# Optimization experiments

Measured on AMD Instinct MI355X. Metric: run time of the kernel, lower is better.

The kernel has to match this reference:

```python
import jax, jax.numpy as jnp
import numpy as np

B, S, H = 2, 2048, 2048
NH, NKV, HD = 16, 4, 128
NEG = -1e9


def rotate_half(x):
    x1, x2 = x[..., : x.shape[-1] // 2], x[..., x.shape[-1] // 2 :]
    return jnp.concatenate((-x2, x1), axis=-1)


def setup_inputs() -> dict:
    key = jax.random.key(0)
    ks = jax.random.split(key, 6)
    hidden_states = jax.random.normal(ks[0], (B, S, H), dtype=jnp.float32)
    # causal additive mask [B, 1, S, S]
    causal = jnp.tril(jnp.ones((S, S), dtype=bool))
    attention_mask = jnp.where(causal, 0.0, NEG).astype(jnp.float32)
    attention_mask = jnp.broadcast_to(attention_mask, (B, 1, S, S))
    # rotary embeddings, base 10000
    inv_freq = 1.0 / (10000.0 ** (np.arange(0, HD, 2, dtype=np.float32) / HD))
    pos = np.arange(S, dtype=np.float32)
    freqs = np.outer(pos, inv_freq)  # [S, HD/2]
    emb = np.concatenate([freqs, freqs], axis=-1)  # [S, HD]
    cos = jnp.broadcast_to(jnp.asarray(np.cos(emb)), (B, S, HD))
    sin = jnp.broadcast_to(jnp.asarray(np.sin(emb)), (B, S, HD))
    sc = 0.02
    Wq = jax.random.normal(ks[1], (H, NH * HD), dtype=jnp.float32) * sc
    Wk = jax.random.normal(ks[2], (H, NKV * HD), dtype=jnp.float32) * sc
    Wv = jax.random.normal(ks[3], (H, NKV * HD), dtype=jnp.float32) * sc
    Wo = jax.random.normal(ks[4], (H, H), dtype=jnp.float32) * sc
    return {"hidden_states": hidden_states, "attention_mask": attention_mask,
            "cos": cos, "sin": sin, "Wq": Wq, "Wk": Wk, "Wv": Wv, "Wo": Wo}


def reference(hidden_states, attention_mask, cos, sin, Wq, Wk, Wv, Wo):
    b, s, _ = hidden_states.shape
    # projections -> [b, heads, s, hd]
    q = (hidden_states @ Wq).reshape(b, s, NH, HD).transpose(0, 2, 1, 3)
    k = (hidden_states @ Wk).reshape(b, s, NKV, HD).transpose(0, 2, 1, 3)
    v = (hidden_states @ Wv).reshape(b, s, NKV, HD).transpose(0, 2, 1, 3)
    # RoPE (cos/sin unsqueezed at dim 1)
    c, sn = cos[:, None], sin[:, None]
    q = q * c + rotate_half(q) * sn
    k = k * c + rotate_half(k) * sn
    # GQA repeat_kv: [b, nkv, s, hd] -> [b, nh, s, hd]
    n_rep = NH // NKV
    k = jnp.repeat(k, n_rep, axis=1)
    v = jnp.repeat(v, n_rep, axis=1)
    scores = jnp.einsum("bhqd,bhkd->bhqk", q, k) / jnp.sqrt(jnp.float32(HD))
    scores = scores + attention_mask
    probs = jax.nn.softmax(scores.astype(jnp.float32), axis=-1).astype(q.dtype)
    out = jnp.einsum("bhqk,bhkd->bhqd", probs, v)
    out = out.transpose(0, 2, 1, 3).reshape(b, s, NH * HD)
    return out @ Wo
```

## Files before the change

kernel.cpp:

```cpp
#include <hip/hip_runtime.h>
#include <hip/hip_bf16.h>

typedef __bf16 bf16;
typedef __bf16 bf16x4 __attribute__((ext_vector_type(4)));
typedef __bf16 bf16x8 __attribute__((ext_vector_type(8)));
typedef float f32x4 __attribute__((ext_vector_type(4)));

__device__ __forceinline__ void gload_lds16(const void* g, void* l) {
  __builtin_amdgcn_global_load_lds((__attribute__((address_space(1))) void*)(g),
                                   (__attribute__((address_space(3))) void*)(l), 16, 0, 0);
}
__device__ __forceinline__ float fexp2(float x) {
  float r;
  asm volatile("v_exp_f32 %0, %1" : "=v"(r) : "v"(x));
  return r;
}

__global__ void k_diag(float* __restrict__ o, float v) { o[threadIdx.x] = v; }

__global__ void k_cvt_bf16(const float* __restrict__ x, bf16* __restrict__ y, int n4) {
  int i = blockIdx.x * blockDim.x + threadIdx.x;
  if (i < n4) {
    float4 v = reinterpret_cast<const float4*>(x)[i];
    bf16x4 o = {(bf16)v.x, (bf16)v.y, (bf16)v.z, (bf16)v.w};
    reinterpret_cast<bf16x4*>(y)[i] = o;
  }
}

__global__ void k_transpose_w(const float* __restrict__ W, bf16* __restrict__ Wt, int K, int N) {
  __shared__ float tile[32][33];
  int kb = blockIdx.x * 32, nb = blockIdx.y * 32;
  int tx = threadIdx.x & 31, ty = threadIdx.x >> 5;
#pragma unroll
  for (int i = 0; i < 32; i += 8)
    tile[ty + i][tx] = W[(size_t)(kb + ty + i) * N + nb + tx];
  __syncthreads();
#pragma unroll
  for (int i = 0; i < 32; i += 8)
    Wt[(size_t)(nb + ty + i) * K + kb + tx] = (bf16)tile[tx][ty + i];
}

__global__ void k_transpose_v(const bf16* __restrict__ KVb, bf16* __restrict__ Vt) {
  __shared__ bf16 tile[32][34];
  constexpr int S = 2048;
  int sb = blockIdx.x * 32, db = blockIdx.y * 32, bh = blockIdx.z;
  int b = bh >> 2, kvh = bh & 3;
  int tx = threadIdx.x & 31, ty = threadIdx.x >> 5;
  const bf16* src = KVb + (size_t)b * S * 1024 + 512 + kvh * 128;
#pragma unroll
  for (int i = 0; i < 32; i += 8)
    tile[ty + i][tx] = src[(size_t)(sb + ty + i) * 1024 + db + tx];
  __syncthreads();
  bf16* dst = Vt + (size_t)bh * 128 * S;
#pragma unroll
  for (int i = 0; i < 32; i += 8)
    dst[(size_t)(db + ty + i) * S + sb + tx] = tile[tx][ty + i];
}

template <typename OT>
__global__ __launch_bounds__(256) void k_gemm(const bf16* __restrict__ A, const bf16* __restrict__ Bt,
                                              OT* __restrict__ C, int M, int N, int Kd) {
  __shared__ __align__(16) bf16 sA[2][128 * 32];
  __shared__ __align__(16) bf16 sB[2][128 * 32];
  const int t = threadIdx.x;
  const int w = t >> 6, l = t & 63;
  const int lr = l & 15, lk = l >> 4;
  const int gx = gridDim.x, nwg = gx * gridDim.y;
  const int flat = blockIdx.y * gx + blockIdx.x;
  const int vid = (flat & 7) * (nwg >> 3) + (flat >> 3);
  const int m0 = (vid % gx) * 128, n0 = (vid / gx) * 128;
  const int wm = (w >> 1) * 64, wn = (w & 1) * 64;
  const bf16* ga = A + (size_t)(m0 + (t >> 2)) * Kd + (t & 3) * 8;
  const bf16* gb = Bt + (size_t)(n0 + (t >> 2)) * Kd + (t & 3) * 8;
  const size_t rowskip = (size_t)64 * Kd;
  auto stage = [&](int k0, int buf) {
    gload_lds16(ga + k0, sA[buf] + w * 512);
    gload_lds16(ga + rowskip + k0, sA[buf] + w * 512 + 2048);
    gload_lds16(gb + k0, sB[buf] + w * 512);
    gload_lds16(gb + rowskip + k0, sB[buf] + w * 512 + 2048);
  };
  f32x4 acc[4][4] = {};
  stage(0, 0);
  __syncthreads();
  int cur = 0;
  for (int k0 = 0; k0 < Kd; k0 += 32) {
    if (k0 + 32 < Kd) stage(k0 + 32, cur ^ 1);
    bf16x8 af[4], bfr[4];
#pragma unroll
    for (int i = 0; i < 4; ++i)
      af[i] = *reinterpret_cast<const bf16x8*>(sA[cur] + (wm + i * 16 + lr) * 32 + lk * 8);
#pragma unroll
    for (int j = 0; j < 4; ++j)
      bfr[j] = *reinterpret_cast<const bf16x8*>(sB[cur] + (wn + j * 16 + lr) * 32 + lk * 8);
#pragma unroll
    for (int i = 0; i < 4; ++i)
#pragma unroll
      for (int j = 0; j < 4; ++j)
        acc[i][j] = __builtin_amdgcn_mfma_f32_16x16x32_bf16(af[i], bfr[j], acc[i][j], 0, 0, 0);
    __syncthreads();
    cur ^= 1;
  }
#pragma unroll
  for (int i = 0; i < 4; ++i)
#pragma unroll
    for (int j = 0; j < 4; ++j)
#pragma unroll
      for (int r = 0; r < 4; ++r) {
        int row = m0 + wm + i * 16 + lk * 4 + r;
        int col = n0 + wn + j * 16 + lr;
        if constexpr (sizeof(OT) == 4)
          C[(size_t)row * N + col] = acc[i][j][r];
        else
          C[(size_t)row * N + col] = (bf16)acc[i][j][r];
      }
}

__global__ void k_rope(bf16* __restrict__ X, const float* __restrict__ cs, const float* __restrict__ sn,
                       int nh, int rowstride, float scale, int total) {
  int idx = blockIdx.x * blockDim.x + threadIdx.x;
  if (idx >= total) return;
  int d = idx & 63;
  int th = idx >> 6;
  int h = th % nh;
  int tok = th / nh;
  size_t base = (size_t)tok * rowstride + h * 128;
  float c = cs[tok * 128 + d], s = sn[tok * 128 + d];
  float x1 = (float)X[base + d];
  float x2 = (float)X[base + d + 64];
  X[base + d] = (bf16)((x1 * c - x2 * s) * scale);
  X[base + d + 64] = (bf16)((x2 * c + x1 * s) * scale);
}

__global__ __launch_bounds__(256) void k_attn(const bf16* __restrict__ Q, const bf16* __restrict__ KV,
                                              const bf16* __restrict__ Vt, bf16* __restrict__ O) {
  constexpr int S = 2048, NH = 16, HD = 128, QSTR = NH * HD, KVSTR = 1024;
  __shared__ __align__(16) bf16 sK[2][64 * 128];
  __shared__ __align__(16) bf16 sV[2][128 * 64];
  __shared__ __align__(16) bf16 sP[4][16][72];
  const int bid = blockIdx.x;
  const int vid = (bid & 7) * 64 + (bid >> 3);
  const int p = vid & 15, bh = vid >> 4;
  const int h = bh & 15, b = bh >> 4;
  const int t = threadIdx.x, w = t >> 6, l = t & 63;
  const int lr = l & 15, lk = l >> 4;
  const int kvh = h >> 2;
  const int swz = (lr & 7) << 4;

  const char* kbase = (const char*)(KV + (size_t)b * S * KVSTR + kvh * HD);
  const int krow_l = w * 16 + (l >> 4);
  const int kcol_l = (l & 15) << 4;
  const char* vtbase = (const char*)(Vt + (size_t)(b * 4 + kvh) * HD * S);
  const int vrow_l = w * 32 + (l >> 3);
  const int vcol_l = (l & 7) << 4;
  char* sKb = (char*)sK;
  char* sVb = (char*)sV;
  auto stage = [&](int kvb, int buf) {
#pragma unroll
    for (int c = 0; c < 4; ++c) {
      const int krow = krow_l + c * 4;
      gload_lds16(kbase + (size_t)(kvb + krow) * 2048 + (kcol_l ^ ((krow & 7) << 4)),
                  sKb + buf * 16384 + (w * 4 + c) * 1024);
      const int vrow = vrow_l + c * 8;
      gload_lds16(vtbase + (size_t)vrow * (S * 2) + kvb * 2 + (vcol_l ^ ((vrow & 7) << 4)),
                  sVb + buf * 16384 + (w * 4 + c) * 1024);
    }
  };

  for (int seg = 0; seg < 2; ++seg) {
    const int qtl = seg ? (31 - p) : p;
    const int qw = qtl * 64 + w * 16;
    const int ntiles = qtl + 1;
    int cur = 0;
    stage(0, 0);
    const bf16* Qp = Q + (size_t)(b * S + qw + lr) * QSTR + h * HD + lk * 8;
    bf16x8 qf[4];
#pragma unroll
    for (int i = 0; i < 4; ++i) qf[i] = *reinterpret_cast<const bf16x8*>(Qp + i * 32);
    f32x4 oacc[8] = {};
    float mrow[4] = {-3e38f, -3e38f, -3e38f, -3e38f};
    float lsum[4] = {0.f, 0.f, 0.f, 0.f};
    __syncthreads();
    for (int tt = 0; tt < ntiles; ++tt) {
      const int kvb = tt * 64;
      if (tt + 1 < ntiles) stage(kvb + 64, cur ^ 1);
      const char* sKc = sKb + cur * 16384;
      const char* sVc = sVb + cur * 16384;
      float pm[4][4];
#pragma unroll
      for (int c = 0; c < 4; ++c) {
        f32x4 s4 = {};
#pragma unroll
        for (int kf = 0; kf < 4; ++kf) {
          bf16x8 kf8 = *reinterpret_cast<const bf16x8*>(
              sKc + (c * 16 + lr) * 256 + (((kf * 64) + (lk << 4)) ^ swz));
          s4 = __builtin_amdgcn_mfma_f32_16x16x32_bf16(qf[kf], kf8, s4, 0, 0, 0);
        }
#pragma unroll
        for (int r = 0; r < 4; ++r) pm[c][r] = s4[r];
      }
      if (tt == ntiles - 1) {
#pragma unroll
        for (int c = 0; c < 4; ++c) {
          const int col = kvb + c * 16 + lr;
#pragma unroll
          for (int r = 0; r < 4; ++r)
            if (col > qw + lk * 4 + r) pm[c][r] = -3e38f;
        }
      }
      float pmax[4];
#pragma unroll
      for (int r = 0; r < 4; ++r)
        pmax[r] = fmaxf(fmaxf(pm[0][r], pm[1][r]), fmaxf(pm[2][r], pm[3][r]));
      bool hi = (pmax[0] > mrow[0] + 8.f) | (pmax[1] > mrow[1] + 8.f) |
                (pmax[2] > mrow[2] + 8.f) | (pmax[3] > mrow[3] + 8.f);
      if (__any(hi)) {
        float mx[4];
#pragma unroll
        for (int r = 0; r < 4; ++r) mx[r] = pmax[r];
#pragma unroll
        for (int off = 1; off < 16; off <<= 1)
#pragma unroll
          for (int r = 0; r < 4; ++r) mx[r] = fmaxf(mx[r], __shfl_xor(mx[r], off));
#pragma unroll
        for (int r = 0; r < 4; ++r) {
          float mn = fmaxf(mrow[r], mx[r]);
          float fac = fexp2(mrow[r] - mn);
          mrow[r] = mn;
          lsum[r] *= fac;
#pragma unroll
          for (int ch = 0; ch < 8; ++ch) oacc[ch][r] *= fac;
        }
      }
#pragma unroll
      for (int c = 0; c < 4; ++c)
#pragma unroll
        for (int r = 0; r < 4; ++r) pm[c][r] = fexp2(pm[c][r] - mrow[r]);
#pragma unroll
      for (int r = 0; r < 4; ++r)
        lsum[r] += (pm[0][r] + pm[1][r]) + (pm[2][r] + pm[3][r]);
#pragma unroll
      for (int c = 0; c < 4; ++c)
#pragma unroll
        for (int r = 0; r < 4; ++r) sP[w][lk * 4 + r][c * 16 + lr] = (bf16)pm[c][r];
      bf16x8 pf0 = *reinterpret_cast<const bf16x8*>(&sP[w][lr][lk * 8]);
      bf16x8 pf1 = *reinterpret_cast<const bf16x8*>(&sP[w][lr][32 + lk * 8]);
#pragma unroll
      for (int ch = 0; ch < 8; ++ch) {
        bf16x8 vf0 = *reinterpret_cast<const bf16x8*>(
            sVc + (ch * 16 + lr) * 128 + ((lk << 4) ^ swz));
        oacc[ch] = __builtin_amdgcn_mfma_f32_16x16x32_bf16(pf0, vf0, oacc[ch], 0, 0, 0);
        bf16x8 vf1 = *reinterpret_cast<const bf16x8*>(
            sVc + (ch * 16 + lr) * 128 + ((64 + (lk << 4)) ^ swz));
        oacc[ch] = __builtin_amdgcn_mfma_f32_16x16x32_bf16(pf1, vf1, oacc[ch], 0, 0, 0);
      }
      __syncthreads();
      cur ^= 1;
    }
#pragma unroll
    for (int off = 1; off < 16; off <<= 1)
#pragma unroll
      for (int r = 0; r < 4; ++r) lsum[r] += __shfl_xor(lsum[r], off);
    float inv[4];
#pragma unroll
    for (int r = 0; r < 4; ++r) inv[r] = 1.0f / lsum[r];
    bf16* Op = O + (size_t)(b * S + qw) * QSTR + h * HD;
#pragma unroll
    for (int ch = 0; ch < 8; ++ch)
#pragma unroll
      for (int r = 0; r < 4; ++r)
        Op[(size_t)(lk * 4 + r) * QSTR + ch * 16 + lr] = (bf16)(oacc[ch][r] * inv[r]);
  }
}

extern "C" void kernel_launch(void* const* d_in, const int* in_sizes, int n_in,
                              void* d_out, int out_size, void* d_ws, size_t ws_size,
                              hipStream_t stream) {
  const float* hs = (const float*)d_in[0];
  const float* cosb = (const float*)d_in[2];
  const float* sinb = (const float*)d_in[3];
  const float* Wq = (const float*)d_in[4];
  const float* Wk = (const float*)d_in[5];
  const float* Wv = (const float*)d_in[6];
  const float* Wo = (const float*)d_in[7];
  float* out = (float*)d_out;

  constexpr int B = 2, S = 2048, H = 2048, NH = 16, NKV = 4, HD = 128;
  constexpr int T = B * S;
  constexpr size_t MB = 1024 * 1024;

  const size_t ws_need = 24 * MB;
  if (ws_size < ws_need) {
    k_diag<<<1, 64, 0, stream>>>(out, 1000.0f + (float)(ws_size / MB));
    return;
  }
  bf16* Xb = (bf16*)d_ws;
  bf16* Wt = (bf16*)((char*)d_ws + 16 * MB);
  bf16* Ob = Xb;
  bf16* Qb = (bf16*)d_out;
  bf16* KVb = (bf16*)((char*)d_out + 16 * MB);
  bf16* Vtb = (bf16*)((char*)d_out + 24 * MB);

  k_cvt_bf16<<<T * H / 4 / 256, 256, 0, stream>>>(hs, Xb, T * H / 4);

  k_transpose_w<<<dim3(H / 32, NH * HD / 32), 256, 0, stream>>>(Wq, Wt, H, NH * HD);
  k_gemm<bf16><<<dim3(T / 128, NH * HD / 128), 256, 0, stream>>>(Xb, Wt, Qb, T, NH * HD, H);

  k_transpose_w<<<dim3(H / 32, NKV * HD / 32), 256, 0, stream>>>(Wk, Wt, H, NKV * HD);
  k_transpose_w<<<dim3(H / 32, NKV * HD / 32), 256, 0, stream>>>(Wv, Wt + (size_t)(NKV * HD) * H, H, NKV * HD);
  k_gemm<bf16><<<dim3(T / 128, 1024 / 128), 256, 0, stream>>>(Xb, Wt, KVb, T, 1024, H);

  k_transpose_v<<<dim3(S / 32, HD / 32, B * NKV), 256, 0, stream>>>(KVb, Vtb);

  const float qscale = 0.12751743f;
  k_rope<<<(T * NH * 64) / 256, 256, 0, stream>>>(Qb, cosb, sinb, NH, NH * HD, qscale, T * NH * 64);
  k_rope<<<(T * NKV * 64) / 256, 256, 0, stream>>>(KVb, cosb, sinb, NKV, 1024, 1.0f, T * NKV * 64);

  k_attn<<<512, 256, 0, stream>>>(Qb, KVb, Vtb, Ob);

  k_transpose_w<<<dim3(H / 32, H / 32), 256, 0, stream>>>(Wo, Wt, H, H);
  k_gemm<float><<<dim3(T / 128, H / 128), 256, 0, stream>>>(Ob, Wt, out, T, H, H);
}
```

Baseline: 255.9 us.

## Use 8-wave deeper-pipelined GEMM and register-resident transposed attention softmax

Replaces the 4-wave 128x128 GEMM with an 8-wave 128x256/256x128 tile kernel. It uses a 4-slot half-K LDS ring with swizzled layout, explicit vmcnt waits and raw barriers, and setprio around the MFMA block. The attention kernel computes S^T (K as A operand) so each lane owns one query row, which reduces row max and sum to two cross-lane shuffles. P is passed to the PV MFMA through packed bf16 register shuffles instead of an LDS round trip. This trades more shuffle and select instructions, plus higher register pressure in the larger GEMM tiles, for fewer LDS accesses and better latency hiding.

```diff
diff --git a/kernel.cpp b/kernel.cpp
--- a/kernel.cpp
+++ b/kernel.cpp
@@ -15,6 +15,12 @@
   asm volatile("v_exp_f32 %0, %1" : "=v"(r) : "v"(x));
   return r;
 }
+__device__ __forceinline__ unsigned cvt_pk_bf16(float lo, float hi) {
+  unsigned r;
+  asm("v_cvt_pk_bf16_f32 %0, %1, %2" : "=v"(r) : "v"(lo), "v"(hi));
+  return r;
+}
+#define S_WAITCNT_VM(n) asm volatile("s_waitcnt vmcnt(" #n ")" ::: "memory")
 
 __global__ void k_diag(float* __restrict__ o, float v) { o[threadIdx.x] = v; }
 
@@ -57,48 +63,67 @@
     dst[(size_t)(db + ty + i) * S + sb + tx] = tile[tx][ty + i];
 }
 
-template <typename OT>
-__global__ __launch_bounds__(256) void k_gemm(const bf16* __restrict__ A, const bf16* __restrict__ Bt,
-                                              OT* __restrict__ C, int M, int N, int Kd) {
-  __shared__ __align__(16) bf16 sA[2][128 * 32];
-  __shared__ __align__(16) bf16 sB[2][128 * 32];
-  const int t = threadIdx.x;
-  const int w = t >> 6, l = t & 63;
+template <int BM, int BN, int WM, int WN, typename OT>
+__global__ __launch_bounds__(512) void k_gemm8(const bf16* __restrict__ A, const bf16* __restrict__ Bt,
+                                               OT* __restrict__ C, int N, int Kd) {
+  constexpr int AS = BM / 16;
+  constexpr int TS = (BM + BN) / 16;
+  __shared__ __align__(16) bf16 sAB[4][TS * 512];
+  const int t = threadIdx.x, w = t >> 6, l = t & 63;
   const int lr = l & 15, lk = l >> 4;
   const int gx = gridDim.x, nwg = gx * gridDim.y;
   const int flat = blockIdx.y * gx + blockIdx.x;
   const int vid = (flat & 7) * (nwg >> 3) + (flat >> 3);
-  const int m0 = (vid % gx) * 128, n0 = (vid / gx) * 128;
-  const int wm = (w >> 1) * 64, wn = (w & 1) * 64;
-  const bf16* ga = A + (size_t)(m0 + (t >> 2)) * Kd + (t & 3) * 8;
-  const bf16* gb = Bt + (size_t)(n0 + (t >> 2)) * Kd + (t & 3) * 8;
-  const size_t rowskip = (size_t)64 * Kd;
-  auto stage = [&](int k0, int buf) {
-    gload_lds16(ga + k0, sA[buf] + w * 512);
-    gload_lds16(ga + rowskip + k0, sA[buf] + w * 512 + 2048);
-    gload_lds16(gb + k0, sB[buf] + w * 512);
-    gload_lds16(gb + rowskip + k0, sB[buf] + w * 512 + 2048);
+  const int m0 = (vid % gx) * BM, n0 = (vid / gx) * BN;
+  const int wm = w / WN, wn = w % WN;
+  const int srow = l >> 2;
+  const int lchunk = (l & 3) ^ ((l >> 2) & 3);
+  const int rdoff = lr * 64 + ((lk ^ (lr & 3)) << 4);
+  const int nkt = Kd >> 6;
+  char* lds = (char*)sAB;
+
+  auto stage = [&](int idx) {
+    const int kt = idx >> 1, kh = idx & 1;
+    const int k0 = (kt << 6) + (kh << 5);
+    char* dst = lds + ((((kt & 1) << 1) + kh) * (TS * 1024));
+#pragma unroll
+    for (int u = 0; u < 3; ++u) {
+      const int j = w * 3 + u;
+      const bf16* src = (j < AS)
+          ? A + (size_t)(m0 + j * 16 + srow) * Kd + k0 + lchunk * 8
+          : Bt + (size_t)(n0 + (j - AS) * 16 + srow) * Kd + k0 + lchunk * 8;
+      gload_lds16(src, dst + j * 1024);
+    }
   };
+
   f32x4 acc[4][4] = {};
-  stage(0, 0);
-  __syncthreads();
-  int cur = 0;
-  for (int k0 = 0; k0 < Kd; k0 += 32) {
-    if (k0 + 32 < Kd) stage(k0 + 32, cur ^ 1);
+  stage(0); stage(1); stage(2);
+  const int PL = 2 * nkt;
+  for (int P = 0; P < PL; ++P) {
+    const int rem = PL - 1 - P;
+    if (rem >= 2) { S_WAITCNT_VM(6); }
+    else if (rem == 1) { S_WAITCNT_VM(3); }
+    else { S_WAITCNT_VM(0); }
+    __builtin_amdgcn_sched_barrier(0);
+    __builtin_amdgcn_s_barrier();
+    __builtin_amdgcn_sched_barrier(0);
+    if (P + 3 < PL) stage(P + 3);
+    const char* hb = lds + (((((P >> 1) & 1) << 1) + (P & 1)) * (TS * 1024));
     bf16x8 af[4], bfr[4];
 #pragma unroll
     for (int i = 0; i < 4; ++i)
-      af[i] = *reinterpret_cast<const bf16x8*>(sA[cur] + (wm + i * 16 + lr) * 32 + lk * 8);
+      af[i] = *reinterpret_cast<const bf16x8*>(hb + (wm * 4 + i) * 1024 + rdoff);
 #pragma unroll
     for (int j = 0; j < 4; ++j)
-      bfr[j] = *reinterpret_cast<const bf16x8*>(sB[cur] + (wn + j * 16 + lr) * 32 + lk * 8);
+      bfr[j] = *reinterpret_cast<const bf16x8*>(hb + (AS + wn * 4 + j) * 1024 + rdoff);
+    __builtin_amdgcn_s_setprio(1);
 #pragma unroll
     for (int i = 0; i < 4; ++i)
 #pragma unroll
       for (int j = 0; j < 4; ++j)
         acc[i][j] = __builtin_amdgcn_mfma_f32_16x16x32_bf16(af[i], bfr[j], acc[i][j], 0, 0, 0);
-    __syncthreads();
-    cur ^= 1;
+    __builtin_amdgcn_s_setprio(0);
+    __builtin_amdgcn_sched_barrier(0);
   }
 #pragma unroll
   for (int i = 0; i < 4; ++i)
@@ -106,8 +131,8 @@
     for (int j = 0; j < 4; ++j)
 #pragma unroll
       for (int r = 0; r < 4; ++r) {
-        int row = m0 + wm + i * 16 + lk * 4 + r;
-        int col = n0 + wn + j * 16 + lr;
+        int row = m0 + wm * 64 + i * 16 + lk * 4 + r;
+        int col = n0 + wn * 64 + j * 16 + lr;
         if constexpr (sizeof(OT) == 4)
           C[(size_t)row * N + col] = acc[i][j][r];
         else
@@ -136,7 +161,6 @@
   constexpr int S = 2048, NH = 16, HD = 128, QSTR = NH * HD, KVSTR = 1024;
   __shared__ __align__(16) bf16 sK[2][64 * 128];
   __shared__ __align__(16) bf16 sV[2][128 * 64];
-  __shared__ __align__(16) bf16 sP[4][16][72];
   const int bid = blockIdx.x;
   const int vid = (bid & 7) * 64 + (bid >> 3);
   const int p = vid & 15, bh = vid >> 4;
@@ -165,6 +189,10 @@
                   sVb + buf * 16384 + (w * 4 + c) * 1024);
     }
   };
+  const int fsrc = (l & 48) | (((l >> 4) & 3) << 2);
+  const int sA = (l & 15) | ((l << 1) & 32);
+  const int sB = sA | 16;
+  const bool sel = (l & 32) != 0;
 
   for (int seg = 0; seg < 2; ++seg) {
     const int qtl = seg ? (31 - p) : p;
@@ -177,8 +205,7 @@
 #pragma unroll
     for (int i = 0; i < 4; ++i) qf[i] = *reinterpret_cast<const bf16x8*>(Qp + i * 32);
     f32x4 oacc[8] = {};
-    float mrow[4] = {-3e38f, -3e38f, -3e38f, -3e38f};
-    float lsum[4] = {0.f, 0.f, 0.f, 0.f};
+    float mrow = -3e38f, lsum = 0.f;
     __syncthreads();
     for (int tt = 0; tt < ntiles; ++tt) {
       const int kvb = tt * 64;
@@ -193,82 +220,88 @@
         for (int kf = 0; kf < 4; ++kf) {
           bf16x8 kf8 = *reinterpret_cast<const bf16x8*>(
               sKc + (c * 16 + lr) * 256 + (((kf * 64) + (lk << 4)) ^ swz));
-          s4 = __builtin_amdgcn_mfma_f32_16x16x32_bf16(qf[kf], kf8, s4, 0, 0, 0);
+          s4 = __builtin_amdgcn_mfma_f32_16x16x32_bf16(kf8, qf[kf], s4, 0, 0, 0);
         }
 #pragma unroll
         for (int r = 0; r < 4; ++r) pm[c][r] = s4[r];
       }
       if (tt == ntiles - 1) {
-#pragma unroll
-        for (int c = 0; c < 4; ++c) {
-          const int col = kvb + c * 16 + lr;
+        const int q = qw + lr;
+#pragma unroll
+        for (int c = 0; c < 4; ++c)
 #pragma unroll
           for (int r = 0; r < 4; ++r)
-            if (col > qw + lk * 4 + r) pm[c][r] = -3e38f;
+            if (kvb + c * 16 + lk * 4 + r > q) pm[c][r] = -3e38f;
+      }
+      float m01 = fmaxf(fmaxf(pm[0][0], pm[0][1]), fmaxf(pm[0][2], pm[0][3]));
+      float m23 = fmaxf(fmaxf(pm[1][0], pm[1][1]), fmaxf(pm[1][2], pm[1][3]));
+      float m45 = fmaxf(fmaxf(pm[2][0], pm[2][1]), fmaxf(pm[2][2], pm[2][3]));
+      float m67 = fmaxf(fmaxf(pm[3][0], pm[3][1]), fmaxf(pm[3][2], pm[3][3]));
+      float rowmax = fmaxf(fmaxf(m01, m23), fmaxf(m45, m67));
+      rowmax = fmaxf(rowmax, __shfl_xor(rowmax, 16));
+      rowmax = fmaxf(rowmax, __shfl_xor(rowmax, 32));
+      if (__any(rowmax > mrow + 8.f)) {
+        float mn = fmaxf(mrow, rowmax);
+        float fac = fexp2(mrow - mn);
+        mrow = mn;
+        lsum *= fac;
+        float f0 = __shfl(fac, fsrc), f1 = __shfl(fac, fsrc + 1);
+        float f2 = __shfl(fac, fsrc + 2), f3 = __shfl(fac, fsrc + 3);
+#pragma unroll
+        for (int ch = 0; ch < 8; ++ch) {
+          oacc[ch][0] *= f0; oacc[ch][1] *= f1; oacc[ch][2] *= f2; oacc[ch][3] *= f3;
         }
       }
-      float pmax[4];
-#pragma unroll
-      for (int r = 0; r < 4; ++r)
-        pmax[r] = fmaxf(fmaxf(pm[0][r], pm[1][r]), fmaxf(pm[2][r], pm[3][r]));
-      bool hi = (pmax[0] > mrow[0] + 8.f) | (pmax[1] > mrow[1] + 8.f) |
-                (pmax[2] > mrow[2] + 8.f) | (pmax[3] > mrow[3] + 8.f);
-      if (__any(hi)) {
-        float mx[4];
-#pragma unroll
-        for (int r = 0; r < 4; ++r) mx[r] = pmax[r];
-#pragma unroll
-        for (int off = 1; off < 16; off <<= 1)
-#pragma unroll
-          for (int r = 0; r < 4; ++r) mx[r] = fmaxf(mx[r], __shfl_xor(mx[r], off));
-#pragma unroll
-        for (int r = 0; r < 4; ++r) {
-          float mn = fmaxf(mrow[r], mx[r]);
-          float fac = fexp2(mrow[r] - mn);
-          mrow[r] = mn;
-          lsum[r] *= fac;
-#pragma unroll
-          for (int ch = 0; ch < 8; ++ch) oacc[ch][r] *= fac;
-        }
-      }
 #pragma unroll
       for (int c = 0; c < 4; ++c)
 #pragma unroll
-        for (int r = 0; r < 4; ++r) pm[c][r] = fexp2(pm[c][r] - mrow[r]);
-#pragma unroll
-      for (int r = 0; r < 4; ++r)
-        lsum[r] += (pm[0][r] + pm[1][r]) + (pm[2][r] + pm[3][r]);
-#pragma unroll
-      for (int c = 0; c < 4; ++c)
-#pragma unroll
-        for (int r = 0; r < 4; ++r) sP[w][lk * 4 + r][c * 16 + lr] = (bf16)pm[c][r];
-      bf16x8 pf0 = *reinterpret_cast<const bf16x8*>(&sP[w][lr][lk * 8]);
-      bf16x8 pf1 = *reinterpret_cast<const bf16x8*>(&sP[w][lr][32 + lk * 8]);
+        for (int r = 0; r < 4; ++r) pm[c][r] = fexp2(pm[c][r] - mrow);
+      lsum += ((pm[0][0] + pm[0][1]) + (pm[0][2] + pm[0][3])) +
+              ((pm[1][0] + pm[1][1]) + (pm[1][2] + pm[1][3])) +
+              ((pm[2][0] + pm[2][1]) + (pm[2][2] + pm[2][3])) +
+              ((pm[3][0] + pm[3][1]) + (pm[3][2] + pm[3][3]));
+      unsigned u0l = cvt_pk_bf16(pm[0][0], pm[0][1]), u0h = cvt_pk_bf16(pm[0][2], pm[0][3]);
+      unsigned u1l = cvt_pk_bf16(pm[1][0], pm[1][1]), u1h = cvt_pk_bf16(pm[1][2], pm[1][3]);
+      unsigned u2l = cvt_pk_bf16(pm[2][0], pm[2][1]), u2h = cvt_pk_bf16(pm[2][2], pm[2][3]);
+      unsigned u3l = cvt_pk_bf16(pm[3][0], pm[3][1]), u3h = cvt_pk_bf16(pm[3][2], pm[3][3]);
+      unsigned a0l = __shfl(u0l, sA), a0h = __shfl(u0h, sA);
+      unsigned a1l = __shfl(u1l, sA), a1h = __shfl(u1h, sA);
+      unsigned a2l = __shfl(u2l, sA), a2h = __shfl(u2h, sA);
+      unsigned a3l = __shfl(u3l, sA), a3h = __shfl(u3h, sA);
+      unsigned b0l = __shfl(u0l, sB), b0h = __shfl(u0h, sB);
+      unsigned b1l = __shfl(u1l, sB), b1h = __shfl(u1h, sB);
+      unsigned b2l = __shfl(u2l, sB), b2h = __shfl(u2h, sB);
+      unsigned b3l = __shfl(u3l, sB), b3h = __shfl(u3h, sB);
+      union U8 { unsigned u[4]; bf16x8 v; } pa0, pa1;
+      pa0.u[0] = sel ? a1l : a0l;  pa0.u[1] = sel ? a1h : a0h;
+      pa0.u[2] = sel ? b1l : b0l;  pa0.u[3] = sel ? b1h : b0h;
+      pa1.u[0] = sel ? a3l : a2l;  pa1.u[1] = sel ? a3h : a2h;
+      pa1.u[2] = sel ? b3l : b2l;  pa1.u[3] = sel ? b3h : b2h;
 #pragma unroll
       for (int ch = 0; ch < 8; ++ch) {
         bf16x8 vf0 = *reinterpret_cast<const bf16x8*>(
             sVc + (ch * 16 + lr) * 128 + ((lk << 4) ^ swz));
-        oacc[ch] = __builtin_amdgcn_mfma_f32_16x16x32_bf16(pf0, vf0, oacc[ch], 0, 0, 0);
+        oacc[ch] = __builtin_amdgcn_mfma_f32_16x16x32_bf16(pa0.v, vf0, oacc[ch], 0, 0, 0);
         bf16x8 vf1 = *reinterpret_cast<const bf16x8*>(
             sVc + (ch * 16 + lr) * 128 + ((64 + (lk << 4)) ^ swz));
-        oacc[ch] = __builtin_amdgcn_mfma_f32_16x16x32_bf16(pf1, vf1, oacc[ch], 0, 0, 0);
+        oacc[ch] = __builtin_amdgcn_mfma_f32_16x16x32_bf16(pa1.v, vf1, oacc[ch], 0, 0, 0);
       }
       __syncthreads();
       cur ^= 1;
     }
-#pragma unroll
-    for (int off = 1; off < 16; off <<= 1)
-#pragma unroll
-      for (int r = 0; r < 4; ++r) lsum[r] += __shfl_xor(lsum[r], off);
-    float inv[4];
-#pragma unroll
-    for (int r = 0; r < 4; ++r) inv[r] = 1.0f / lsum[r];
+    lsum += __shfl_xor(lsum, 16);
+    lsum += __shfl_xor(lsum, 32);
+    float inv = 1.0f / lsum;
+    float i0 = __shfl(inv, fsrc), i1 = __shfl(inv, fsrc + 1);
+    float i2 = __shfl(inv, fsrc + 2), i3 = __shfl(inv, fsrc + 3);
     bf16* Op = O + (size_t)(b * S + qw) * QSTR + h * HD;
 #pragma unroll
-    for (int ch = 0; ch < 8; ++ch)
-#pragma unroll
-      for (int r = 0; r < 4; ++r)
-        Op[(size_t)(lk * 4 + r) * QSTR + ch * 16 + lr] = (bf16)(oacc[ch][r] * inv[r]);
+    for (int ch = 0; ch < 8; ++ch) {
+      Op[(size_t)(lk * 4 + 0) * QSTR + ch * 16 + lr] = (bf16)(oacc[ch][0] * i0);
+      Op[(size_t)(lk * 4 + 1) * QSTR + ch * 16 + lr] = (bf16)(oacc[ch][1] * i1);
+      Op[(size_t)(lk * 4 + 2) * QSTR + ch * 16 + lr] = (bf16)(oacc[ch][2] * i2);
+      Op[(size_t)(lk * 4 + 3) * QSTR + ch * 16 + lr] = (bf16)(oacc[ch][3] * i3);
+    }
   }
 }
 
@@ -303,11 +336,11 @@
   k_cvt_bf16<<<T * H / 4 / 256, 256, 0, stream>>>(hs, Xb, T * H / 4);
 
   k_transpose_w<<<dim3(H / 32, NH * HD / 32), 256, 0, stream>>>(Wq, Wt, H, NH * HD);
-  k_gemm<bf16><<<dim3(T / 128, NH * HD / 128), 256, 0, stream>>>(Xb, Wt, Qb, T, NH * HD, H);
+  k_gemm8<128, 256, 2, 4, bf16><<<dim3(32, 8), 512, 0, stream>>>(Xb, Wt, Qb, NH * HD, H);
 
   k_transpose_w<<<dim3(H / 32, NKV * HD / 32), 256, 0, stream>>>(Wk, Wt, H, NKV * HD);
   k_transpose_w<<<dim3(H / 32, NKV * HD / 32), 256, 0, stream>>>(Wv, Wt + (size_t)(NKV * HD) * H, H, NKV * HD);
-  k_gemm<bf16><<<dim3(T / 128, 1024 / 128), 256, 0, stream>>>(Xb, Wt, KVb, T, 1024, H);
+  k_gemm8<256, 128, 4, 2, bf16><<<dim3(16, 8), 512, 0, stream>>>(Xb, Wt, KVb, 1024, H);
 
   k_transpose_v<<<dim3(S / 32, HD / 32, B * NKV), 256, 0, stream>>>(KVb, Vtb);
 
@@ -318,5 +351,5 @@
   k_attn<<<512, 256, 0, stream>>>(Qb, KVb, Vtb, Ob);
 
   k_transpose_w<<<dim3(H / 32, H / 32), 256, 0, stream>>>(Wo, Wt, H, H);
-  k_gemm<float><<<dim3(T / 128, H / 128), 256, 0, stream>>>(Ob, Wt, out, T, H, H);
-}
+  k_gemm8<128, 256, 2, 4, float><<<dim3(32, 8), 512, 0, stream>>>(Ob, Wt, out, H, H);
+}
```

After: 238.8 us. 1.07x faster.
